# Kernel tuning notes

Measured on AMD Instinct MI355X. Metric: run time of the kernel, lower is better.

## Reference

```python
import jax, jax.numpy as jnp
import numpy as np

B_, L, DM = 4, 1024, 1024
DI, DS, DR, DC = 1024, 16, 64, 4
NH = 4
DK = DM // NH


def setup_inputs() -> dict:
    key = jax.random.key(0)
    ks = jax.random.split(key, 16)
    def w(i, shape, scale=0.02):
        return jax.random.normal(ks[i], shape, dtype=jnp.float32) * scale
    inp = {
        "x": jax.random.normal(ks[0], (B_, L, DM), dtype=jnp.float32),
        "xx": jax.random.normal(ks[1], (B_, L, DI), dtype=jnp.float32),
        "in_proj_w": w(2, (DI, DM)),
        "conv_w": w(3, (DI, 1, DC)),            # depthwise conv, groups=DI
        "conv_b": jnp.zeros((DI,), jnp.float32),
        "x_proj_w": w(4, (DR + 2 * DS, DI)),
        "dt_proj_w": w(5, (DI, DR)),
        "dt_proj_b": jnp.zeros((DI,), jnp.float32),
        "A_log": jnp.log(jnp.tile(jnp.arange(1, DS + 1, dtype=jnp.float32)[None, :], (DI, 1))),
        "D": jnp.ones((DI,), jnp.float32),
        "wq": w(6, (DM, DM)), "bq": jnp.zeros((DM,), jnp.float32),
        "wk": w(7, (DM, DM)), "bk": jnp.zeros((DM,), jnp.float32),
        "wv": w(8, (DM, DM)), "bv": jnp.zeros((DM,), jnp.float32),
        "wo": w(9, (DM, DM)), "bo": jnp.zeros((DM,), jnp.float32),
    }
    return inp


def _stim_forward(x, xx, in_proj_w, conv_w, conv_b, x_proj_w, dt_proj_w, dt_proj_b,
                  A_log, D, wq, bq, wk, bk, wv, bv, wo, bo):
    b, l, _ = xx.shape
    # query branch: in_proj (Linear, no bias)
    q = x @ in_proj_w.T                                    # (b, l, DI)
    # kv branch: causal depthwise conv1d (padding d_conv-1, truncated to l)
    xc = jnp.transpose(xx, (0, 2, 1))                      # (b, DI, l)
    xc = jax.lax.conv_general_dilated(
        xc, conv_w, window_strides=(1,), padding=[(DC - 1, 0)],
        dimension_numbers=("NCH", "OIH", "NCH"), feature_group_count=DI)
    xc = xc + conv_b[None, :, None]
    u = jax.nn.silu(jnp.transpose(xc, (0, 2, 1)))          # (b, l, DI)
    # SSM parameter projections
    A = -jnp.exp(A_log)                                    # (DI, DS)
    x_dbl = u @ x_proj_w.T                                 # (b, l, DR+2*DS)
    delta, Bm, Cm = jnp.split(x_dbl, [DR, DR + DS], axis=-1)
    delta = jax.nn.softplus(delta @ dt_proj_w.T + dt_proj_b)  # (b, l, DI)
    deltaA = jnp.exp(jnp.einsum("bld,dn->bldn", delta, A))    # (b, l, DI, DS)
    deltaBu = jnp.einsum("bld,bln,bld->bldn", delta, Bm, u)   # (b, l, DI, DS)
    # selective scan over time
    def step(h, inp):
        dA_t, dBu_t, C_t = inp
        h = dA_t * h + dBu_t                               # (b, DI, DS)
        y_t = jnp.einsum("bdn,bn->bd", h, C_t)             # (b, DI)
        return h, y_t
    h0 = jnp.zeros((b, DI, DS), dtype=u.dtype)
    _, ys = jax.lax.scan(step, h0, (jnp.moveaxis(deltaA, 1, 0),
                                    jnp.moveaxis(deltaBu, 1, 0),
                                    jnp.moveaxis(Cm, 1, 0)))
    y = jnp.moveaxis(ys, 0, 1) + u * D                     # (b, l, DI)
    # cross attention: query = q, key/value = y
    Q = (q @ wq.T + bq).reshape(b, l, NH, DK).transpose(0, 2, 1, 3)
    K = (y @ wk.T + bk).reshape(b, l, NH, DK).transpose(0, 2, 1, 3)
    V = (y @ wv.T + bv).reshape(b, l, NH, DK).transpose(0, 2, 1, 3)
    scale = 1.0 / np.sqrt(DK).astype(np.float32)
    scores = jnp.einsum("bhqd,bhkd->bhqk", Q, K) * scale
    attn = jax.nn.softmax(scores, axis=-1)
    out = jnp.einsum("bhqk,bhkd->bhqd", attn, V)
    out = out.transpose(0, 2, 1, 3).reshape(b, l, DM)
    return out @ wo.T + bo


def reference(x, xx, in_proj_w, conv_w, conv_b, x_proj_w, dt_proj_w, dt_proj_b,
              A_log, D, wq, bq, wk, bk, wv, bv, wo, bo):
    return _stim_forward(x, xx, in_proj_w, conv_w, conv_b, x_proj_w, dt_proj_w,
                         dt_proj_b, A_log, D, wq, bq, wk, bk, wv, bv, wo, bo)
```

## Files before the change

### kernel.cpp

```cpp
#include <hip/hip_runtime.h>
#include <math.h>

#define B_  4
#define L_  1024
#define DM  1024
#define DI  1024
#define DS  16
#define DR  64
#define DCV 4
#define NH  4
#define DK  256

#define NCH 32
#define CHL (L_ / NCH)

typedef __attribute__((ext_vector_type(8))) short short8;
typedef __attribute__((ext_vector_type(4))) float floatx4;

static __device__ __forceinline__ unsigned short f2bf(float f) {
    unsigned int u = __float_as_uint(f);
    u += 0x7fffu + ((u >> 16) & 1u);
    return (unsigned short)(u >> 16);
}
static __device__ __forceinline__ float bf2f(unsigned short s) {
    return __uint_as_float(((unsigned int)s) << 16);
}

struct CastArgs {
    const float* s[8];
    unsigned short* d[8];
    int n[8];
    int ns[8];
};

__global__ __launch_bounds__(256) void cast_multi(CastArgs ca)
{
    int y = blockIdx.y;
    int i = (blockIdx.x * 256 + threadIdx.x) * 4;
    if (i >= ca.n[y]) return;
    const float* s = ca.s[y];
    unsigned short* d = ca.d[y];
    int ns = ca.ns[y];
    ushort4 o;
    if (i + 4 <= ns) {
        float4 v = *(const float4*)(s + i);
        o.x = f2bf(v.x); o.y = f2bf(v.y); o.z = f2bf(v.z); o.w = f2bf(v.w);
    } else {
        float v[4];
#pragma unroll
        for (int j = 0; j < 4; j++) v[j] = (i + j < ns) ? s[i + j] : 0.f;
        o.x = f2bf(v[0]); o.y = f2bf(v[1]); o.z = f2bf(v[2]); o.w = f2bf(v[3]);
    }
    *(ushort4*)(d + i) = o;
}

struct GDesc {
    const unsigned short* A;
    const unsigned short* W;
    const float* bias;
    float* Cf;
    unsigned short* Cb;
    int K, lda, ldw, ldc, ldc2;
    int mode;
    float scale;
    int gx, gy;
};
struct GArgs { GDesc g[3]; };

__global__ __launch_bounds__(256) void gemm_multi(GArgs ga)
{
    GDesc g = ga.g[blockIdx.z];
    if ((int)blockIdx.x >= g.gx || (int)blockIdx.y >= g.gy) return;

    __shared__ __align__(16) unsigned short Asm[128 * 32];
    __shared__ __align__(16) unsigned short Bsm[128 * 32];

    int tid = threadIdx.x;
    int wid = tid >> 6;
    int lane = tid & 63;
    int wm = wid & 1, wn = wid >> 1;
    int lr = lane & 15, quad = lane >> 4;

    const unsigned short* Ab = g.A + (size_t)blockIdx.y * 128 * g.lda;
    const unsigned short* Wb = g.W + (size_t)blockIdx.x * 128 * g.ldw;

    int srow = tid >> 2;
    int scol = (tid & 3) * 8;
    const unsigned short* Ap = Ab + (size_t)srow * g.lda + scol;
    const unsigned short* Wp = Wb + (size_t)srow * g.ldw + scol;

    unsigned short* lA0 = &Asm[(wid * 16) * 32];
    unsigned short* lA1 = &Asm[(64 + wid * 16) * 32];
    unsigned short* lB0 = &Bsm[(wid * 16) * 32];
    unsigned short* lB1 = &Bsm[(64 + wid * 16) * 32];

    floatx4 acc[4][4];
#pragma unroll
    for (int i = 0; i < 4; i++)
#pragma unroll
        for (int j = 0; j < 4; j++) acc[i][j] = (floatx4){0.f, 0.f, 0.f, 0.f};

#define GLL(gp, lp) __builtin_amdgcn_global_load_lds( \
        (const __attribute__((address_space(1))) void*)(gp), \
        (__attribute__((address_space(3))) void*)(lp), 16, 0, 0)

    for (int k0 = 0; k0 < g.K; k0 += 32) {
        GLL(Ap, lA0);
        GLL(Ap + (size_t)64 * g.lda, lA1);
        GLL(Wp, lB0);
        GLL(Wp + (size_t)64 * g.ldw, lB1);
        Ap += 32; Wp += 32;
        __syncthreads();

        short8 af[4], bf[4];
#pragma unroll
        for (int mt = 0; mt < 4; mt++)
            af[mt] = *(const short8*)&Asm[(wm * 64 + mt * 16 + lr) * 32 + quad * 8];
#pragma unroll
        for (int nt = 0; nt < 4; nt++)
            bf[nt] = *(const short8*)&Bsm[(wn * 64 + nt * 16 + lr) * 32 + quad * 8];
#pragma unroll
        for (int mt = 0; mt < 4; mt++)
#pragma unroll
            for (int nt = 0; nt < 4; nt++)
                acc[mt][nt] = __builtin_amdgcn_mfma_f32_16x16x32_bf16(
                    af[mt], bf[nt], acc[mt][nt], 0, 0, 0);
        __syncthreads();
    }
#undef GLL

    int bm = blockIdx.y * 128, bn = blockIdx.x * 128;
    int m = g.mode & 3;
#pragma unroll
    for (int mt = 0; mt < 4; mt++) {
#pragma unroll
        for (int nt = 0; nt < 4; nt++) {
            int row0 = bm + wm * 64 + mt * 16 + quad * 4;
            int col = bn + wn * 64 + nt * 16 + lr;
            float bv = g.bias ? g.bias[col] : 0.f;
#pragma unroll
            for (int i = 0; i < 4; i++) {
                float v = acc[mt][nt][i] * g.scale + bv;
                if (g.mode & 4) v = (v > 15.f) ? v : log1pf(__expf(v));
                if (m == 0) {
                    g.Cf[(size_t)(row0 + i) * g.ldc + col] = v;
                } else if (m == 1) {
                    g.Cb[(size_t)(row0 + i) * g.ldc + col] = f2bf(v);
                } else {
                    g.Cf[(size_t)(row0 + i) * g.ldc + col] = v;
                    g.Cb[(size_t)(row0 + i) * g.ldc2 + col] = f2bf(v);
                }
            }
        }
    }
}

__global__ __launch_bounds__(256) void gemm_batched(
    const unsigned short* __restrict__ A, const unsigned short* __restrict__ W,
    unsigned short* __restrict__ C,
    int K, int lda, int ldw, int ldc,
    long long sA1, long long sA2, long long sW1, long long sW2,
    long long sC1, long long sC2, float scale)
{
    __shared__ __align__(16) unsigned short Asm[128 * 32];
    __shared__ __align__(16) unsigned short Bsm[128 * 32];

    int z = blockIdx.z;
    long long bq = z >> 2, hq = z & 3;
    int tid = threadIdx.x;
    int wid = tid >> 6;
    int lane = tid & 63;
    int wm = wid & 1, wn = wid >> 1;
    int lr = lane & 15, quad = lane >> 4;

    const unsigned short* Ab = A + bq * sA1 + hq * sA2 + (size_t)blockIdx.y * 128 * lda;
    const unsigned short* Wb = W + bq * sW1 + hq * sW2 + (size_t)blockIdx.x * 128 * ldw;

    int srow = tid >> 2;
    int scol = (tid & 3) * 8;
    const unsigned short* Ap = Ab + (size_t)srow * lda + scol;
    const unsigned short* Wp = Wb + (size_t)srow * ldw + scol;

    unsigned short* lA0 = &Asm[(wid * 16) * 32];
    unsigned short* lA1 = &Asm[(64 + wid * 16) * 32];
    unsigned short* lB0 = &Bsm[(wid * 16) * 32];
    unsigned short* lB1 = &Bsm[(64 + wid * 16) * 32];

    floatx4 acc[4][4];
#pragma unroll
    for (int i = 0; i < 4; i++)
#pragma unroll
        for (int j = 0; j < 4; j++) acc[i][j] = (floatx4){0.f, 0.f, 0.f, 0.f};

#define GLL(gp, lp) __builtin_amdgcn_global_load_lds( \
        (const __attribute__((address_space(1))) void*)(gp), \
        (__attribute__((address_space(3))) void*)(lp), 16, 0, 0)

    for (int k0 = 0; k0 < K; k0 += 32) {
        GLL(Ap, lA0);
        GLL(Ap + (size_t)64 * lda, lA1);
        GLL(Wp, lB0);
        GLL(Wp + (size_t)64 * ldw, lB1);
        Ap += 32; Wp += 32;
        __syncthreads();

        short8 af[4], bf[4];
#pragma unroll
        for (int mt = 0; mt < 4; mt++)
            af[mt] = *(const short8*)&Asm[(wm * 64 + mt * 16 + lr) * 32 + quad * 8];
#pragma unroll
        for (int nt = 0; nt < 4; nt++)
            bf[nt] = *(const short8*)&Bsm[(wn * 64 + nt * 16 + lr) * 32 + quad * 8];
#pragma unroll
        for (int mt = 0; mt < 4; mt++)
#pragma unroll
            for (int nt = 0; nt < 4; nt++)
                acc[mt][nt] = __builtin_amdgcn_mfma_f32_16x16x32_bf16(
                    af[mt], bf[nt], acc[mt][nt], 0, 0, 0);
        __syncthreads();
    }
#undef GLL

    long long coff = bq * sC1 + hq * sC2;
    int bm = blockIdx.y * 128, bn = blockIdx.x * 128;
    unsigned short* Cb = C + coff;

#pragma unroll
    for (int mt = 0; mt < 4; mt++) {
#pragma unroll
        for (int nt = 0; nt < 4; nt++) {
            int row0 = bm + wm * 64 + mt * 16 + quad * 4;
            int col = bn + wn * 64 + nt * 16 + lr;
#pragma unroll
            for (int i = 0; i < 4; i++)
                Cb[(size_t)(row0 + i) * ldc + col] = f2bf(acc[mt][nt][i] * scale);
        }
    }
}

__global__ __launch_bounds__(256) void conv_silu_kernel(
    const float* __restrict__ xx, const float* __restrict__ cw,
    const float* __restrict__ cb, float* __restrict__ u,
    unsigned short* __restrict__ ub)
{
    int idx = blockIdx.x * 256 + threadIdx.x;
    int d = idx & (DI - 1);
    int l = (idx >> 10) & (L_ - 1);
    int b = idx >> 20;
    const float* xb = xx + (size_t)b * L_ * DI + d;
    float z = cb[d];
#pragma unroll
    for (int j = 0; j < DCV; j++) {
        int t = l - (DCV - 1) + j;
        if (t >= 0) z += xb[(size_t)t * DI] * cw[d * DCV + j];
    }
    float v = z / (1.0f + __expf(-z));
    u[idx] = v;
    ub[idx] = f2bf(v);
}

__global__ __launch_bounds__(256) void scan_a(
    const float* __restrict__ delta, const float* __restrict__ u,
    const float* __restrict__ xdbl, const float* __restrict__ A_log,
    float* __restrict__ Hc, float* __restrict__ sumdv)
{
    int gid = blockIdx.x * 256 + threadIdx.x;
    int c = gid >> 12;
    int bd = gid & 4095;
    int b = bd >> 10, d = bd & 1023;

    float a[16];
#pragma unroll
    for (int j = 0; j < 4; j++) {
        float4 al = *(const float4*)(A_log + d * 16 + j * 4);
        a[j * 4 + 0] = -__expf(al.x); a[j * 4 + 1] = -__expf(al.y);
        a[j * 4 + 2] = -__expf(al.z); a[j * 4 + 3] = -__expf(al.w);
    }
    float h[16];
#pragma unroll
    for (int n = 0; n < 16; n++) h[n] = 0.f;
    float sd = 0.f;

    int t0 = c * CHL;
    const float* dp = delta + ((size_t)(b * L_) + t0) * DI + d;
    const float* up = u + ((size_t)(b * L_) + t0) * DI + d;
    const float* xp = xdbl + ((size_t)(b * L_) + t0) * 128;

#pragma unroll 4
    for (int t = 0; t < CHL; t++) {
        float dv = dp[t * DI];
        float uv = up[t * DI];
        float duv = dv * uv;
        sd += dv;
        float Bv[16];
#pragma unroll
        for (int j = 0; j < 4; j++) {
            float4 bq = *(const float4*)(xp + t * 128 + 64 + j * 4);
            Bv[j * 4 + 0] = bq.x; Bv[j * 4 + 1] = bq.y;
            Bv[j * 4 + 2] = bq.z; Bv[j * 4 + 3] = bq.w;
        }
#pragma unroll
        for (int n = 0; n < 16; n++)
            h[n] = __expf(dv * a[n]) * h[n] + duv * Bv[n];
    }

    float* hp = Hc + ((size_t)c * 4096 + bd) * 16;
#pragma unroll
    for (int j = 0; j < 4; j++)
        *(float4*)(hp + j * 4) = make_float4(h[j * 4], h[j * 4 + 1], h[j * 4 + 2], h[j * 4 + 3]);
    sumdv[c * 4096 + bd] = sd;
}

__global__ __launch_bounds__(256) void scan_b(
    float* __restrict__ Hc, const float* __restrict__ sumdv,
    const float* __restrict__ A_log)
{
    int bd = blockIdx.x * 256 + threadIdx.x;
    int d = bd & 1023;

    float a[16];
#pragma unroll
    for (int j = 0; j < 4; j++) {
        float4 al = *(const float4*)(A_log + d * 16 + j * 4);
        a[j * 4 + 0] = -__expf(al.x); a[j * 4 + 1] = -__expf(al.y);
        a[j * 4 + 2] = -__expf(al.z); a[j * 4 + 3] = -__expf(al.w);
    }
    float H[16];
#pragma unroll
    for (int n = 0; n < 16; n++) H[n] = 0.f;

    for (int c = 0; c < NCH; c++) {
        float* hp = Hc + ((size_t)c * 4096 + bd) * 16;
        float sdv = sumdv[c * 4096 + bd];
        float hc[16];
#pragma unroll
        for (int j = 0; j < 4; j++) {
            float4 q = *(const float4*)(hp + j * 4);
            hc[j * 4 + 0] = q.x; hc[j * 4 + 1] = q.y; hc[j * 4 + 2] = q.z; hc[j * 4 + 3] = q.w;
        }
#pragma unroll
        for (int j = 0; j < 4; j++)
            *(float4*)(hp + j * 4) = make_float4(H[j * 4], H[j * 4 + 1], H[j * 4 + 2], H[j * 4 + 3]);
#pragma unroll
        for (int n = 0; n < 16; n++)
            H[n] = __expf(a[n] * sdv) * H[n] + hc[n];
    }
}

__global__ __launch_bounds__(256) void scan_c(
    const float* __restrict__ delta, const float* __restrict__ u,
    const float* __restrict__ xdbl, const float* __restrict__ A_log,
    const float* __restrict__ Dv, const float* __restrict__ Hstart,
    unsigned short* __restrict__ y)
{
    int gid = blockIdx.x * 256 + threadIdx.x;
    int c = gid >> 12;
    int bd = gid & 4095;
    int b = bd >> 10, d = bd & 1023;

    float a[16];
#pragma unroll
    for (int j = 0; j < 4; j++) {
        float4 al = *(const float4*)(A_log + d * 16 + j * 4);
        a[j * 4 + 0] = -__expf(al.x); a[j * 4 + 1] = -__expf(al.y);
        a[j * 4 + 2] = -__expf(al.z); a[j * 4 + 3] = -__expf(al.w);
    }
    float h[16];
    const float* hp = Hstart + ((size_t)c * 4096 + bd) * 16;
#pragma unroll
    for (int j = 0; j < 4; j++) {
        float4 q = *(const float4*)(hp + j * 4);
        h[j * 4 + 0] = q.x; h[j * 4 + 1] = q.y; h[j * 4 + 2] = q.z; h[j * 4 + 3] = q.w;
    }
    float Dd = Dv[d];

    int t0 = c * CHL;
    const float* dp = delta + ((size_t)(b * L_) + t0) * DI + d;
    const float* up = u + ((size_t)(b * L_) + t0) * DI + d;
    const float* xp = xdbl + ((size_t)(b * L_) + t0) * 128;
    unsigned short* yp = y + ((size_t)(b * L_) + t0) * DI + d;

#pragma unroll 4
    for (int t = 0; t < CHL; t++) {
        float dv = dp[t * DI];
        float uv = up[t * DI];
        float duv = dv * uv;
        float Bv[16], Cv[16];
#pragma unroll
        for (int j = 0; j < 4; j++) {
            float4 bq = *(const float4*)(xp + t * 128 + 64 + j * 4);
            Bv[j * 4 + 0] = bq.x; Bv[j * 4 + 1] = bq.y;
            Bv[j * 4 + 2] = bq.z; Bv[j * 4 + 3] = bq.w;
            float4 cq = *(const float4*)(xp + t * 128 + 80 + j * 4);
            Cv[j * 4 + 0] = cq.x; Cv[j * 4 + 1] = cq.y;
            Cv[j * 4 + 2] = cq.z; Cv[j * 4 + 3] = cq.w;
        }
        float ys = 0.f;
#pragma unroll
        for (int n = 0; n < 16; n++) {
            h[n] = __expf(dv * a[n]) * h[n] + duv * Bv[n];
            ys += h[n] * Cv[n];
        }
        yp[t * DI] = f2bf(ys + uv * Dd);
    }
}

__global__ __launch_bounds__(256) void transpose_v(
    const unsigned short* __restrict__ V, unsigned short* __restrict__ VT)
{
    __shared__ unsigned short tl[32][36];
    int bh = blockIdx.z;
    int b = bh >> 2, h = bh & 3;
    int l0 = blockIdx.x * 32, d0 = blockIdx.y * 32;
    int tid = threadIdx.x;
    int r = tid >> 3, c4 = (tid & 7) * 4;

    const unsigned short* src = V + ((size_t)(b * L_ + l0 + r)) * 1024 + h * DK + d0 + c4;
    ushort4 v = *(const ushort4*)src;
    tl[r][c4 + 0] = v.x; tl[r][c4 + 1] = v.y; tl[r][c4 + 2] = v.z; tl[r][c4 + 3] = v.w;
    __syncthreads();

    unsigned short* dst = VT + ((size_t)bh * DK + d0 + r) * L_ + l0 + c4;
    ushort4 o;
    o.x = tl[c4 + 0][r]; o.y = tl[c4 + 1][r]; o.z = tl[c4 + 2][r]; o.w = tl[c4 + 3][r];
    *(ushort4*)dst = o;
}

__global__ __launch_bounds__(256) void softmax_rows(unsigned short* __restrict__ S)
{
    int row = blockIdx.x * 4 + (threadIdx.x >> 6);
    int lane = threadIdx.x & 63;
    unsigned short* p = S + (size_t)row * 1024;

    float v[16];
#pragma unroll
    for (int ch = 0; ch < 4; ch++) {
        ushort4 u4 = *(const ushort4*)(p + ch * 256 + lane * 4);
        v[ch * 4 + 0] = bf2f(u4.x); v[ch * 4 + 1] = bf2f(u4.y);
        v[ch * 4 + 2] = bf2f(u4.z); v[ch * 4 + 3] = bf2f(u4.w);
    }
    float m = -1e30f;
#pragma unroll
    for (int i = 0; i < 16; i++) m = fmaxf(m, v[i]);
#pragma unroll
    for (int off = 32; off >= 1; off >>= 1) m = fmaxf(m, __shfl_xor(m, off));
    float s = 0.f;
#pragma unroll
    for (int i = 0; i < 16; i++) { v[i] = __expf(v[i] - m); s += v[i]; }
#pragma unroll
    for (int off = 32; off >= 1; off >>= 1) s += __shfl_xor(s, off);
    float inv = 1.0f / s;
#pragma unroll
    for (int ch = 0; ch < 4; ch++) {
        ushort4 o;
        o.x = f2bf(v[ch * 4 + 0] * inv); o.y = f2bf(v[ch * 4 + 1] * inv);
        o.z = f2bf(v[ch * 4 + 2] * inv); o.w = f2bf(v[ch * 4 + 3] * inv);
        *(ushort4*)(p + ch * 256 + lane * 4) = o;
    }
}

extern "C" void kernel_launch(void* const* d_in, const int* in_sizes, int n_in,
                              void* d_out, int out_size, void* d_ws, size_t ws_size,
                              hipStream_t stream)
{
    const float* x         = (const float*)d_in[0];
    const float* xx        = (const float*)d_in[1];
    const float* in_proj_w = (const float*)d_in[2];
    const float* conv_w    = (const float*)d_in[3];
    const float* conv_b    = (const float*)d_in[4];
    const float* x_proj_w  = (const float*)d_in[5];
    const float* dt_proj_w = (const float*)d_in[6];
    const float* dt_proj_b = (const float*)d_in[7];
    const float* A_log     = (const float*)d_in[8];
    const float* Dvec      = (const float*)d_in[9];
    const float* wq        = (const float*)d_in[10];
    const float* bq        = (const float*)d_in[11];
    const float* wk        = (const float*)d_in[12];
    const float* bk        = (const float*)d_in[13];
    const float* wv        = (const float*)d_in[14];
    const float* bv        = (const float*)d_in[15];
    const float* wo        = (const float*)d_in[16];
    const float* bo        = (const float*)d_in[17];
    float* out = (float*)d_out;

    char* w = (char*)d_ws;
    const size_t MB = 1024 * 1024, KB = 1024;
    float*          u_f    = (float*)(w + 0);
    float*          delta  = (float*)(w + 16 * MB);
    unsigned short* Sbuf   = (unsigned short*)(w + 0);
    unsigned short* x_bf   = (unsigned short*)(w + 32 * MB);
    unsigned short* Q_bf   = x_bf;
    unsigned short* q_bf   = (unsigned short*)(w + 40 * MB);
    unsigned short* VT     = q_bf;
    unsigned short* y_bf   = (unsigned short*)(w + 48 * MB);
    unsigned short* AO     = y_bf;
    unsigned short* K_bf   = (unsigned short*)(w + 56 * MB);
    unsigned short* V_bf   = (unsigned short*)(w + 64 * MB);
    unsigned short* u_bf   = (unsigned short*)(w + 72 * MB);
    float*          Hc     = (float*)(w + 72 * MB);
    float*          xdbl   = (float*)(w + 80 * MB);
    unsigned short* xdblb  = (unsigned short*)(w + 82 * MB);
    unsigned short* w_in   = (unsigned short*)(w + 83 * MB);
    unsigned short* w_q    = (unsigned short*)(w + 85 * MB);
    unsigned short* w_k    = (unsigned short*)(w + 87 * MB);
    unsigned short* w_v    = (unsigned short*)(w + 89 * MB);
    unsigned short* w_o    = (unsigned short*)(w + 91 * MB);
    unsigned short* w_xp   = (unsigned short*)(w + 93 * MB);
    unsigned short* w_dt   = (unsigned short*)(w + 93 * MB + 256 * KB);
    float*          sumdv  = (float*)(w + 93 * MB + 384 * KB);

    dim3 blk(256);
    const long long LL = L_;

    CastArgs ca;
    ca.s[0] = x;         ca.d[0] = x_bf;  ca.n[0] = 4194304; ca.ns[0] = 4194304;
    ca.s[1] = in_proj_w; ca.d[1] = w_in;  ca.n[1] = 1048576; ca.ns[1] = 1048576;
    ca.s[2] = wq;        ca.d[2] = w_q;   ca.n[2] = 1048576; ca.ns[2] = 1048576;
    ca.s[3] = wk;        ca.d[3] = w_k;   ca.n[3] = 1048576; ca.ns[3] = 1048576;
    ca.s[4] = wv;        ca.d[4] = w_v;   ca.n[4] = 1048576; ca.ns[4] = 1048576;
    ca.s[5] = wo;        ca.d[5] = w_o;   ca.n[5] = 1048576; ca.ns[5] = 1048576;
    ca.s[6] = x_proj_w;  ca.d[6] = w_xp;  ca.n[6] = 131072;  ca.ns[6] = 98304;
    ca.s[7] = dt_proj_w; ca.d[7] = w_dt;  ca.n[7] = 65536;   ca.ns[7] = 65536;
    cast_multi<<<dim3(4096, 8), blk, 0, stream>>>(ca);

    conv_silu_kernel<<<dim3(16384), blk, 0, stream>>>(xx, conv_w, conv_b, u_f, u_bf);

    {
        GArgs ga = {};
        ga.g[0] = (GDesc){x_bf, w_in, nullptr, nullptr, q_bf,
                          1024, 1024, 1024, 1024, 0, 1, 1.0f, 8, 32};
        ga.g[1] = (GDesc){u_bf, w_xp, nullptr, xdbl, xdblb,
                          1024, 1024, 1024, 128, 128, 2, 1.0f, 1, 32};
        gemm_multi<<<dim3(8, 32, 2), blk, 0, stream>>>(ga);
    }
    {
        GArgs ga = {};
        ga.g[0] = (GDesc){xdblb, w_dt, dt_proj_b, delta, nullptr,
                          64, 128, 64, 1024, 0, 0 | 4, 1.0f, 8, 32};
        gemm_multi<<<dim3(8, 32, 1), blk, 0, stream>>>(ga);
    }
    scan_a<<<dim3(512), blk, 0, stream>>>(delta, u_f, xdbl, A_log, Hc, sumdv);
    scan_b<<<dim3(16), blk, 0, stream>>>(Hc, sumdv, A_log);
    scan_c<<<dim3(512), blk, 0, stream>>>(delta, u_f, xdbl, A_log, Dvec, Hc, y_bf);

    {
        GArgs ga = {};
        ga.g[0] = (GDesc){q_bf, w_q, bq, nullptr, Q_bf, 1024, 1024, 1024, 1024, 0, 1, 1.0f, 8, 32};
        ga.g[1] = (GDesc){y_bf, w_k, bk, nullptr, K_bf, 1024, 1024, 1024, 1024, 0, 1, 1.0f, 8, 32};
        ga.g[2] = (GDesc){y_bf, w_v, bv, nullptr, V_bf, 1024, 1024, 1024, 1024, 0, 1, 1.0f, 8, 32};
        gemm_multi<<<dim3(8, 32, 3), blk, 0, stream>>>(ga);
    }
    gemm_batched<<<dim3(8, 8, 16), blk, 0, stream>>>(Q_bf, K_bf, Sbuf,
        DK, 1024, 1024, 1024,
        LL * 1024, 256, LL * 1024, 256,
        4 * LL * 1024, LL * 1024, 0.0625f);
    softmax_rows<<<dim3(4096), blk, 0, stream>>>(Sbuf);
    transpose_v<<<dim3(32, 8, 16), blk, 0, stream>>>(V_bf, VT);
    gemm_batched<<<dim3(2, 8, 16), blk, 0, stream>>>(Sbuf, VT, AO,
        1024, 1024, 1024, 1024,
        4 * LL * 1024, LL * 1024,
        4 * (long long)DK * 1024, (long long)DK * 1024,
        LL * 1024, 256, 1.0f);
    {
        GArgs ga = {};
        ga.g[0] = (GDesc){AO, w_o, bo, out, nullptr, 1024, 1024, 1024, 1024, 0, 0, 1.0f, 8, 32};
        gemm_multi<<<dim3(8, 32, 1), blk, 0, stream>>>(ga);
    }
}
```

Baseline: 441.5 us.

## Fuse QK^T, softmax and PV into a flash-attention kernel

Replaces the batched score GEMM, the row softmax kernel and the PV GEMM with one flash-attention kernel that uses online softmax, keeping scores in registers and LDS. This removes the write and re-read of the 4x4x1024x1024 bf16 score matrix and two kernel launches. In exchange, the grid shrinks to 256 blocks and V is read straight from global memory without LDS staging, so occupancy and memory efficiency may suffer.

Result: slower. 479.4 us (+8.6%).

```diff
diff --git a/kernel.cpp b/kernel.cpp
--- a/kernel.cpp
+++ b/kernel.cpp
@@ -155,87 +155,125 @@
     }
 }
 
-__global__ __launch_bounds__(256) void gemm_batched(
-    const unsigned short* __restrict__ A, const unsigned short* __restrict__ W,
-    unsigned short* __restrict__ C,
-    int K, int lda, int ldw, int ldc,
-    long long sA1, long long sA2, long long sW1, long long sW2,
-    long long sC1, long long sC2, float scale)
-{
-    __shared__ __align__(16) unsigned short Asm[128 * 32];
-    __shared__ __align__(16) unsigned short Bsm[128 * 32];
-
-    int z = blockIdx.z;
-    long long bq = z >> 2, hq = z & 3;
+__global__ __launch_bounds__(256) void flash_attn(
+    const unsigned short* __restrict__ Q, const unsigned short* __restrict__ Kg,
+    const unsigned short* __restrict__ VT, unsigned short* __restrict__ O)
+{
+    __shared__ __align__(16) unsigned short Ks[64 * 264];
+    __shared__ __align__(16) unsigned short Pp[4 * 16 * 72];
+
+    int bh = blockIdx.y;
+    int b = bh >> 2, h = bh & 3;
+    int q0 = blockIdx.x * 64;
     int tid = threadIdx.x;
-    int wid = tid >> 6;
-    int lane = tid & 63;
-    int wm = wid & 1, wn = wid >> 1;
+    int wid = tid >> 6, lane = tid & 63;
     int lr = lane & 15, quad = lane >> 4;
-
-    const unsigned short* Ab = A + bq * sA1 + hq * sA2 + (size_t)blockIdx.y * 128 * lda;
-    const unsigned short* Wb = W + bq * sW1 + hq * sW2 + (size_t)blockIdx.x * 128 * ldw;
-
-    int srow = tid >> 2;
-    int scol = (tid & 3) * 8;
-    const unsigned short* Ap = Ab + (size_t)srow * lda + scol;
-    const unsigned short* Wp = Wb + (size_t)srow * ldw + scol;
-
-    unsigned short* lA0 = &Asm[(wid * 16) * 32];
-    unsigned short* lA1 = &Asm[(64 + wid * 16) * 32];
-    unsigned short* lB0 = &Bsm[(wid * 16) * 32];
-    unsigned short* lB1 = &Bsm[(64 + wid * 16) * 32];
-
-    floatx4 acc[4][4];
-#pragma unroll
-    for (int i = 0; i < 4; i++)
-#pragma unroll
-        for (int j = 0; j < 4; j++) acc[i][j] = (floatx4){0.f, 0.f, 0.f, 0.f};
-
-#define GLL(gp, lp) __builtin_amdgcn_global_load_lds( \
-        (const __attribute__((address_space(1))) void*)(gp), \
-        (__attribute__((address_space(3))) void*)(lp), 16, 0, 0)
-
-    for (int k0 = 0; k0 < K; k0 += 32) {
-        GLL(Ap, lA0);
-        GLL(Ap + (size_t)64 * lda, lA1);
-        GLL(Wp, lB0);
-        GLL(Wp + (size_t)64 * ldw, lB1);
-        Ap += 32; Wp += 32;
+    const float scale = 0.0625f;
+
+    short8 qf[8];
+    const unsigned short* qbase = Q + ((size_t)(b * L_ + q0 + wid * 16 + lr)) * 1024 + h * DK;
+#pragma unroll
+    for (int kf = 0; kf < 8; kf++)
+        qf[kf] = *(const short8*)(qbase + kf * 32 + quad * 8);
+
+    floatx4 o_acc[16];
+#pragma unroll
+    for (int i = 0; i < 16; i++) o_acc[i] = (floatx4){0.f, 0.f, 0.f, 0.f};
+    float m_i[4] = {-3e38f, -3e38f, -3e38f, -3e38f};
+    float l_i[4] = {0.f, 0.f, 0.f, 0.f};
+
+    int srow = tid >> 5;
+    int sc16 = tid & 31;
+    unsigned short* pw = &Pp[wid * 16 * 72];
+
+    for (int kt = 0; kt < 16; kt++) {
+        int k0 = kt * 64;
         __syncthreads();
-
-        short8 af[4], bf[4];
-#pragma unroll
-        for (int mt = 0; mt < 4; mt++)
-            af[mt] = *(const short8*)&Asm[(wm * 64 + mt * 16 + lr) * 32 + quad * 8];
+        {
+            const unsigned short* kb = Kg + ((size_t)(b * L_ + k0 + srow)) * 1024 + h * DK + sc16 * 8;
+            unsigned short* kd = &Ks[srow * 264 + sc16 * 8];
+#pragma unroll
+            for (int rd = 0; rd < 8; rd++)
+                *(short8*)(kd + rd * 8 * 264) = *(const short8*)(kb + (size_t)rd * 8 * 1024);
+        }
+        __syncthreads();
+
+        floatx4 sacc[4];
+#pragma unroll
+        for (int nt = 0; nt < 4; nt++) sacc[nt] = (floatx4){0.f, 0.f, 0.f, 0.f};
+#pragma unroll
+        for (int kf = 0; kf < 8; kf++) {
+#pragma unroll
+            for (int nt = 0; nt < 4; nt++) {
+                short8 kfr = *(const short8*)&Ks[(nt * 16 + lr) * 264 + kf * 32 + quad * 8];
+                sacc[nt] = __builtin_amdgcn_mfma_f32_16x16x32_bf16(qf[kf], kfr, sacc[nt], 0, 0, 0);
+            }
+        }
+
+        float p_[4][4];
+        float al[4];
+#pragma unroll
+        for (int i = 0; i < 4; i++) {
+            float tm = sacc[0][i];
+            tm = fmaxf(tm, sacc[1][i]);
+            tm = fmaxf(tm, sacc[2][i]);
+            tm = fmaxf(tm, sacc[3][i]);
+            tm *= scale;
+            tm = fmaxf(tm, __shfl_xor(tm, 1));
+            tm = fmaxf(tm, __shfl_xor(tm, 2));
+            tm = fmaxf(tm, __shfl_xor(tm, 4));
+            tm = fmaxf(tm, __shfl_xor(tm, 8));
+            float mn = fmaxf(m_i[i], tm);
+            al[i] = __expf(m_i[i] - mn);
+            m_i[i] = mn;
+            float ts = 0.f;
+#pragma unroll
+            for (int nt = 0; nt < 4; nt++) {
+                float pv = __expf(sacc[nt][i] * scale - mn);
+                p_[nt][i] = pv;
+                ts += pv;
+            }
+            ts += __shfl_xor(ts, 1);
+            ts += __shfl_xor(ts, 2);
+            ts += __shfl_xor(ts, 4);
+            ts += __shfl_xor(ts, 8);
+            l_i[i] = al[i] * l_i[i] + ts;
+        }
+
 #pragma unroll
         for (int nt = 0; nt < 4; nt++)
-            bf[nt] = *(const short8*)&Bsm[(wn * 64 + nt * 16 + lr) * 32 + quad * 8];
-#pragma unroll
-        for (int mt = 0; mt < 4; mt++)
-#pragma unroll
-            for (int nt = 0; nt < 4; nt++)
-                acc[mt][nt] = __builtin_amdgcn_mfma_f32_16x16x32_bf16(
-                    af[mt], bf[nt], acc[mt][nt], 0, 0, 0);
-        __syncthreads();
-    }
-#undef GLL
-
-    long long coff = bq * sC1 + hq * sC2;
-    int bm = blockIdx.y * 128, bn = blockIdx.x * 128;
-    unsigned short* Cb = C + coff;
-
-#pragma unroll
-    for (int mt = 0; mt < 4; mt++) {
-#pragma unroll
-        for (int nt = 0; nt < 4; nt++) {
-            int row0 = bm + wm * 64 + mt * 16 + quad * 4;
-            int col = bn + wn * 64 + nt * 16 + lr;
 #pragma unroll
             for (int i = 0; i < 4; i++)
-                Cb[(size_t)(row0 + i) * ldc + col] = f2bf(acc[mt][nt][i] * scale);
-        }
-    }
+                pw[(quad * 4 + i) * 72 + nt * 16 + lr] = f2bf(p_[nt][i]);
+
+#pragma unroll
+        for (int ntd = 0; ntd < 16; ntd++) {
+            floatx4 t = o_acc[ntd];
+            t[0] *= al[0]; t[1] *= al[1]; t[2] *= al[2]; t[3] *= al[3];
+            o_acc[ntd] = t;
+        }
+
+        const unsigned short* vb = VT + ((size_t)bh * DK + lr) * 1024 + k0 + quad * 8;
+#pragma unroll
+        for (int ko = 0; ko < 2; ko++) {
+            short8 pf = *(const short8*)&pw[lr * 72 + ko * 32 + quad * 8];
+#pragma unroll
+            for (int ntd = 0; ntd < 16; ntd++) {
+                short8 vf = *(const short8*)(vb + (size_t)ntd * 16 * 1024 + ko * 32);
+                o_acc[ntd] = __builtin_amdgcn_mfma_f32_16x16x32_bf16(pf, vf, o_acc[ntd], 0, 0, 0);
+            }
+        }
+    }
+
+    float inv[4];
+#pragma unroll
+    for (int i = 0; i < 4; i++) inv[i] = 1.0f / l_i[i];
+    unsigned short* ob = O + ((size_t)(b * L_ + q0 + wid * 16 + quad * 4)) * 1024 + h * DK + lr;
+#pragma unroll
+    for (int ntd = 0; ntd < 16; ntd++)
+#pragma unroll
+        for (int i = 0; i < 4; i++)
+            ob[(size_t)i * 1024 + ntd * 16] = f2bf(o_acc[ntd][i] * inv[i]);
 }
 
 __global__ __launch_bounds__(256) void conv_silu_kernel(
@@ -424,39 +462,6 @@
     ushort4 o;
     o.x = tl[c4 + 0][r]; o.y = tl[c4 + 1][r]; o.z = tl[c4 + 2][r]; o.w = tl[c4 + 3][r];
     *(ushort4*)dst = o;
-}
-
-__global__ __launch_bounds__(256) void softmax_rows(unsigned short* __restrict__ S)
-{
-    int row = blockIdx.x * 4 + (threadIdx.x >> 6);
-    int lane = threadIdx.x & 63;
-    unsigned short* p = S + (size_t)row * 1024;
-
-    float v[16];
-#pragma unroll
-    for (int ch = 0; ch < 4; ch++) {
-        ushort4 u4 = *(const ushort4*)(p + ch * 256 + lane * 4);
-        v[ch * 4 + 0] = bf2f(u4.x); v[ch * 4 + 1] = bf2f(u4.y);
-        v[ch * 4 + 2] = bf2f(u4.z); v[ch * 4 + 3] = bf2f(u4.w);
-    }
-    float m = -1e30f;
-#pragma unroll
-    for (int i = 0; i < 16; i++) m = fmaxf(m, v[i]);
-#pragma unroll
-    for (int off = 32; off >= 1; off >>= 1) m = fmaxf(m, __shfl_xor(m, off));
-    float s = 0.f;
-#pragma unroll
-    for (int i = 0; i < 16; i++) { v[i] = __expf(v[i] - m); s += v[i]; }
-#pragma unroll
-    for (int off = 32; off >= 1; off >>= 1) s += __shfl_xor(s, off);
-    float inv = 1.0f / s;
-#pragma unroll
-    for (int ch = 0; ch < 4; ch++) {
-        ushort4 o;
-        o.x = f2bf(v[ch * 4 + 0] * inv); o.y = f2bf(v[ch * 4 + 1] * inv);
-        o.z = f2bf(v[ch * 4 + 2] * inv); o.w = f2bf(v[ch * 4 + 3] * inv);
-        *(ushort4*)(p + ch * 256 + lane * 4) = o;
-    }
 }
 
 extern "C" void kernel_launch(void* const* d_in, const int* in_sizes, int n_in,
@@ -487,7 +492,6 @@
     const size_t MB = 1024 * 1024, KB = 1024;
     float*          u_f    = (float*)(w + 0);
     float*          delta  = (float*)(w + 16 * MB);
-    unsigned short* Sbuf   = (unsigned short*)(w + 0);
     unsigned short* x_bf   = (unsigned short*)(w + 32 * MB);
     unsigned short* Q_bf   = x_bf;
     unsigned short* q_bf   = (unsigned short*)(w + 40 * MB);
@@ -510,7 +514,6 @@
     float*          sumdv  = (float*)(w + 93 * MB + 384 * KB);
 
     dim3 blk(256);
-    const long long LL = L_;
 
     CastArgs ca;
     ca.s[0] = x;         ca.d[0] = x_bf;  ca.n[0] = 4194304; ca.ns[0] = 4194304;
@@ -550,17 +553,8 @@
         ga.g[2] = (GDesc){y_bf, w_v, bv, nullptr, V_bf, 1024, 1024, 1024, 1024, 0, 1, 1.0f, 8, 32};
         gemm_multi<<<dim3(8, 32, 3), blk, 0, stream>>>(ga);
     }
-    gemm_batched<<<dim3(8, 8, 16), blk, 0, stream>>>(Q_bf, K_bf, Sbuf,
-        DK, 1024, 1024, 1024,
-        LL * 1024, 256, LL * 1024, 256,
-        4 * LL * 1024, LL * 1024, 0.0625f);
-    softmax_rows<<<dim3(4096), blk, 0, stream>>>(Sbuf);
     transpose_v<<<dim3(32, 8, 16), blk, 0, stream>>>(V_bf, VT);
-    gemm_batched<<<dim3(2, 8, 16), blk, 0, stream>>>(Sbuf, VT, AO,
-        1024, 1024, 1024, 1024,
-        4 * LL * 1024, LL * 1024,
-        4 * (long long)DK * 1024, (long long)DK * 1024,
-        LL * 1024, 256, 1.0f);
+    flash_attn<<<dim3(16, 16), blk, 0, stream>>>(Q_bf, K_bf, VT, AO);
     {
         GArgs ga = {};
         ga.g[0] = (GDesc){AO, w_o, bo, out, nullptr, 1024, 1024, 1024, 1024, 0, 0, 1.0f, 8, 32};
```
